# Kernel tuning notes

Measured on AMD Instinct MI355X. Metric: run time of the kernel, lower is better.

The kernel has to match this reference:

```python
import jax, jax.numpy as jnp
import numpy as np

B, T, D, H, K, V = 2, 2048, 2048, 16, 128, 128


def _l2norm(x, eps=1e-12):
    # F.normalize(p=2, dim=-1)
    n = jnp.sqrt(jnp.sum(x * x, axis=-1, keepdims=True))
    return x / jnp.maximum(n, eps)


def setup_inputs() -> dict:
    key = jax.random.key(0)
    ks = jax.random.split(key, 7)
    s = D ** -0.5
    return {
        "x": jax.random.normal(ks[0], (B, T, D), jnp.float32),
        "Wq": jax.random.normal(ks[1], (H * K, D), jnp.float32) * s,
        "Wk": jax.random.normal(ks[2], (H * K, D), jnp.float32) * s,
        "Wv": jax.random.normal(ks[3], (H * V, D), jnp.float32) * s,
        "Wa": jax.random.normal(ks[4], (H, D), jnp.float32) * s,
        "ba": jnp.zeros((H,), jnp.float32),
        "Wb": jax.random.normal(ks[5], (H, D), jnp.float32) * s,
        "bb": jnp.zeros((H,), jnp.float32),
    }


def _forward(x, Wq, Wk, Wv, Wa, ba, Wb, bb):
    Bq, Tq, _ = x.shape
    # projections (nn.Linear: y = x @ W.T)
    q = _l2norm(jnp.einsum('btd,od->bto', x, Wq).reshape(Bq, Tq, H, K))
    k = _l2norm(jnp.einsum('btd,od->bto', x, Wk).reshape(Bq, Tq, H, K))
    v = jnp.einsum('btd,od->bto', x, Wv).reshape(Bq, Tq, H, V)
    alpha = jax.nn.sigmoid(jnp.einsum('btd,hd->bth', x, Wa) + ba)          # [B,T,H] decay in (0,1)
    beta = jax.nn.softplus(jnp.einsum('btd,hd->bth', x, Wb) + bb) * K ** (-0.5)

    # gated delta rule recurrence over time (vectorized over B,H):
    #   S_t = a_t * S_{t-1} (I - b_t k_t k_t^T) + b_t v_t k_t^T ;  o_t = S_t q_t
    def step(S, inp):
        q_t, k_t, v_t, a_t, b_t = inp  # [B,H,K],[B,H,K],[B,H,V],[B,H],[B,H]
        Sd = S * a_t[..., None, None]                              # decay  [B,H,V,K]
        pred = jnp.einsum('bhvk,bhk->bhv', Sd, k_t)                # S k
        u = b_t[..., None] * (v_t - pred)                          # delta update [B,H,V]
        S_new = Sd + u[..., None] * k_t[:, :, None, :]             # rank-1 write
        o_t = jnp.einsum('bhvk,bhk->bhv', S_new, q_t)
        return S_new, o_t

    S0 = jnp.zeros((Bq, H, V, K), x.dtype)
    xs = (q.transpose(1, 0, 2, 3), k.transpose(1, 0, 2, 3),
          v.transpose(1, 0, 2, 3), alpha.transpose(1, 0, 2), beta.transpose(1, 0, 2))
    _, o = jax.lax.scan(step, S0, xs)
    return o.transpose(1, 0, 2, 3)  # [B,T,H,V]


def reference(x, Wq, Wk, Wv, Wa, ba, Wb, bb):
    return _forward(x, Wq, Wk, Wv, Wa, ba, Wb, bb)
```

## Files before the change

kernel.cpp:

```cpp
#include <hip/hip_runtime.h>
#include <math.h>

#define BB 2
#define TT 2048
#define DD 2048
#define HH 16
#define KK 128

typedef _Float16 h4 __attribute__((ext_vector_type(4)));
typedef _Float16 v8h __attribute__((ext_vector_type(8)));
typedef float v4f __attribute__((ext_vector_type(4)));
typedef float f2 __attribute__((ext_vector_type(2)));
typedef unsigned int u2v __attribute__((ext_vector_type(2)));

__global__ __launch_bounds__(256) void gemm_nt3(const float* __restrict__ A,
                                                const float* __restrict__ W0,
                                                const float* __restrict__ W1,
                                                const float* __restrict__ W2,
                                                float* __restrict__ Cbase,
                                                int M, int N, int Kd) {
  __shared__ float As[8][128];
  __shared__ float Bs[8][128];
  const int z = blockIdx.z;
  const float* W = (z == 0) ? W0 : (z == 1) ? W1 : W2;
  float* C = Cbase + (size_t)z * M * N;
  const int tid = threadIdx.x;
  const int bm = blockIdx.y * 128;
  const int bn = blockIdx.x * 128;
  const int lrow = tid >> 1;
  const int lcol = (tid & 1) * 4;
  const int rm = (tid >> 4) * 8;
  const int rn = (tid & 15) * 8;
  const float* Ap = A + (size_t)(bm + lrow) * Kd + lcol;
  const float* Wp = W + (size_t)(bn + lrow) * Kd + lcol;
  float acc[8][8];
#pragma unroll
  for (int i = 0; i < 8; i++)
#pragma unroll
    for (int j = 0; j < 8; j++) acc[i][j] = 0.f;
  float4 av = *(const float4*)Ap;
  float4 wv = *(const float4*)Wp;
  for (int d0 = 0; d0 < Kd; d0 += 8) {
    __syncthreads();
    As[lcol + 0][lrow] = av.x; As[lcol + 1][lrow] = av.y;
    As[lcol + 2][lrow] = av.z; As[lcol + 3][lrow] = av.w;
    Bs[lcol + 0][lrow] = wv.x; Bs[lcol + 1][lrow] = wv.y;
    Bs[lcol + 2][lrow] = wv.z; Bs[lcol + 3][lrow] = wv.w;
    __syncthreads();
    if (d0 + 8 < Kd) {
      av = *(const float4*)(Ap + d0 + 8);
      wv = *(const float4*)(Wp + d0 + 8);
    }
#pragma unroll
    for (int kk = 0; kk < 8; kk++) {
      const float4 a0 = *(const float4*)&As[kk][rm];
      const float4 a1 = *(const float4*)&As[kk][rm + 4];
      const float4 b0 = *(const float4*)&Bs[kk][rn];
      const float4 b1 = *(const float4*)&Bs[kk][rn + 4];
      const float ar[8] = {a0.x, a0.y, a0.z, a0.w, a1.x, a1.y, a1.z, a1.w};
      const float br[8] = {b0.x, b0.y, b0.z, b0.w, b1.x, b1.y, b1.z, b1.w};
#pragma unroll
      for (int i = 0; i < 8; i++)
#pragma unroll
        for (int j = 0; j < 8; j++) acc[i][j] = fmaf(ar[i], br[j], acc[i][j]);
    }
  }
#pragma unroll
  for (int i = 0; i < 8; i++) {
    float* cp = C + (size_t)(bm + rm + i) * N + bn + rn;
    float4 c0 = {acc[i][0], acc[i][1], acc[i][2], acc[i][3]};
    float4 c1 = {acc[i][4], acc[i][5], acc[i][6], acc[i][7]};
    *(float4*)cp = c0;
    *(float4*)(cp + 4) = c1;
  }
}

__global__ __launch_bounds__(256) void convert_f16(
    const float* __restrict__ x, const float* __restrict__ Wq,
    const float* __restrict__ Wk, const float* __restrict__ Wv,
    _Float16* __restrict__ xh, _Float16* __restrict__ Wf) {
  const size_t N4X = (size_t)BB * TT * DD / 4;
  const size_t N4W = (size_t)(HH * KK) * DD / 4;
  const size_t i = (size_t)blockIdx.x * 256 + threadIdx.x;
  if (i < N4X) {
    const float4 v = ((const float4*)x)[i];
    h4 hi;
    hi.x = (_Float16)v.x; hi.y = (_Float16)v.y;
    hi.z = (_Float16)v.z; hi.w = (_Float16)v.w;
    ((h4*)xh)[i] = hi;
  } else {
    const size_t j = i - N4X;
    const float* Ws = (j < N4W) ? Wq : (j < 2 * N4W) ? Wk : Wv;
    const size_t jj = (j < N4W) ? j : (j < 2 * N4W) ? (j - N4W) : (j - 2 * N4W);
    const float4 v = ((const float4*)Ws)[jj];
    h4 hi;
    hi.x = (_Float16)v.x; hi.y = (_Float16)v.y;
    hi.z = (_Float16)v.z; hi.w = (_Float16)v.w;
    ((h4*)Wf)[j] = hi;
  }
}

#define GLDS(gp, lp)                                              \
  __builtin_amdgcn_global_load_lds(                               \
      (const __attribute__((address_space(1))) void*)(gp),        \
      (__attribute__((address_space(3))) void*)(lp), 16, 0, 0)

__global__ __launch_bounds__(256) void gemm_mfma(
    const _Float16* __restrict__ xh, const _Float16* __restrict__ Wf,
    float* __restrict__ Cbase) {
  __shared__ float4 lraw[1024];
  _Float16* Ah = (_Float16*)lraw;
  _Float16* Bs = Ah + 4096;

  const int z = blockIdx.z;
  const _Float16* W = Wf + (size_t)z * DD * (HH * KK);
  float* C = Cbase + (size_t)z * (BB * TT) * (HH * KK);

  const int tid = threadIdx.x;
  const int w = tid >> 6;
  const int lane = tid & 63;
  const int bm = blockIdx.y * 128;
  const int bn = blockIdx.x * 128;
  const int wm = (w & 1) * 64;
  const int wn = (w >> 1) * 64;
  const int m16 = lane & 15;
  const int quad = lane >> 4;

  const _Float16* gA = xh + (size_t)(bm + (tid >> 2)) * DD + (tid & 3) * 8;
  const _Float16* gB = W + (size_t)(bn + (tid >> 2)) * DD + (tid & 3) * 8;
  const int lb = w * 512;

  v4f acc[4][4];
#pragma unroll
  for (int i = 0; i < 4; i++)
#pragma unroll
    for (int j = 0; j < 4; j++) acc[i][j] = (v4f){0.f, 0.f, 0.f, 0.f};

  for (int d0 = 0; d0 < DD; d0 += 32) {
    GLDS(gA + d0, Ah + lb);
    GLDS(gA + d0 + 64 * DD, Ah + 2048 + lb);
    GLDS(gB + d0, Bs + lb);
    GLDS(gB + d0 + 64 * DD, Bs + 2048 + lb);
    __syncthreads();
    v8h ah[4], bw[4];
#pragma unroll
    for (int i = 0; i < 4; i++) {
      ah[i] = *(const v8h*)&Ah[(wm + i * 16 + m16) * 32 + quad * 8];
      bw[i] = *(const v8h*)&Bs[(wn + i * 16 + m16) * 32 + quad * 8];
    }
#pragma unroll
    for (int mi = 0; mi < 4; mi++)
#pragma unroll
      for (int ni = 0; ni < 4; ni++)
        acc[mi][ni] = __builtin_amdgcn_mfma_f32_16x16x32_f16(ah[mi], bw[ni],
                                                             acc[mi][ni], 0, 0, 0);
    __syncthreads();
  }
#pragma unroll
  for (int mi = 0; mi < 4; mi++) {
#pragma unroll
    for (int r = 0; r < 4; r++) {
      float* cp =
          C + (size_t)(bm + wm + mi * 16 + quad * 4 + r) * (HH * KK) + bn + wn + m16;
#pragma unroll
      for (int ni = 0; ni < 4; ni++) cp[ni * 16] = acc[mi][ni][r];
    }
  }
}

__global__ __launch_bounds__(64) void ab_proj(const float* __restrict__ x,
                                              const float* __restrict__ Wa,
                                              const float* __restrict__ ba,
                                              const float* __restrict__ Wb,
                                              const float* __restrict__ bb,
                                              float* __restrict__ abq) {
  const int row = blockIdx.x;
  const int g = blockIdx.y;
  const int h0 = (g & 1) * 8;
  const bool isA = (g < 2);
  const float* W = isA ? Wa : Wb;
  const int lane = threadIdx.x;
  const float* xr = x + (size_t)row * DD;
  float acc[8];
#pragma unroll
  for (int j = 0; j < 8; j++) acc[j] = 0.f;
  for (int d = lane; d < DD; d += 64) {
    const float xv = xr[d];
#pragma unroll
    for (int j = 0; j < 8; j++)
      acc[j] = fmaf(xv, W[(size_t)(h0 + j) * DD + d], acc[j]);
  }
#pragma unroll
  for (int j = 0; j < 8; j++) {
#pragma unroll
    for (int off = 32; off > 0; off >>= 1) acc[j] += __shfl_xor(acc[j], off, 64);
  }
  if (lane == 0) {
    if (isA) {
#pragma unroll
      for (int j = 0; j < 8; j++) {
        const float z = acc[j] + ba[h0 + j];
        abq[((size_t)row * HH + h0 + j) * 4 + 0] = 1.0f / (1.0f + expf(-z));
      }
    } else {
#pragma unroll
      for (int j = 0; j < 8; j++) {
        const float z = acc[j] + bb[h0 + j];
        const float sp = (z > 20.f) ? z : log1pf(expf(z));
        abq[((size_t)row * HH + h0 + j) * 4 + 1] = sp * 0.08838834764831845f;
      }
    }
  }
}

__global__ __launch_bounds__(256) void norm_qk(float* __restrict__ q,
                                               float* __restrict__ k,
                                               float* __restrict__ abq) {
  const int vec = blockIdx.x * 4 + (threadIdx.x >> 6);
  const int l = threadIdx.x & 63;
  float* qp = q + (size_t)vec * 128;
  float* kp = k + (size_t)vec * 128;
  float q0 = qp[l], q1 = qp[l + 64];
  float k0 = kp[l], k1 = kp[l + 64];
  float sq = q0 * q0 + q1 * q1;
  float sk = k0 * k0 + k1 * k1;
#pragma unroll
  for (int off = 32; off > 0; off >>= 1) {
    sq += __shfl_xor(sq, off, 64);
    sk += __shfl_xor(sk, off, 64);
  }
  const float iq = 1.0f / fmaxf(sqrtf(sq), 1e-12f);
  const float ik = 1.0f / fmaxf(sqrtf(sk), 1e-12f);
  q0 *= iq; q1 *= iq; k0 *= ik; k1 *= ik;
  qp[l] = q0; qp[l + 64] = q1;
  kp[l] = k0; kp[l + 64] = k1;
  float pq = q0 * k0 + q1 * k1;
#pragma unroll
  for (int off = 32; off > 0; off >>= 1) pq += __shfl_xor(pq, off, 64);
  if (l == 0) abq[(size_t)vec * 4 + 2] = pq;
}

#define DPP_ADD(x, ctrl)                                                     \
  ((x) + __int_as_float(__builtin_amdgcn_update_dpp(                         \
             0, __float_as_int(x), (ctrl), 0xF, 0xF, true)))

__device__ __forceinline__ float xadd32(float x) {
  const u2v r = __builtin_amdgcn_permlane32_swap(__float_as_uint(x),
                                                 __float_as_uint(x), false,
                                                 false);
  return __uint_as_float(r.x) + __uint_as_float(r.y);
}

#define SBAR() asm volatile("s_barrier" ::: "memory")
#define WAITV(n) asm volatile("s_waitcnt vmcnt(" #n ")" ::: "memory")

#define SCAN_MATH(kc, qc, vc, ac, jj, obname)                                  \
  {                                                                            \
    const f2 ka = {kc.x, kc.y};                                                \
    const f2 kb2 = {kc.z, kc.w};                                               \
    const f2 qa = {qc.x, qc.y};                                                \
    const f2 qb2 = {qc.z, qc.w};                                               \
    const f2 pdk = __builtin_elementwise_fma(Sb, kb2, Sa * ka);                \
    const f2 pdq = __builtin_elementwise_fma(Sb, qb2, Sa * qa);                \
    float dk = pdk.x + pdk.y;                                                  \
    float dq = pdq.x + pdq.y;                                                  \
    dk = DPP_ADD(dk, 0xB1);  dq = DPP_ADD(dq, 0xB1);             \
    dk = DPP_ADD(dk, 0x4E);  dq = DPP_ADD(dq, 0x4E);             \
    dk = DPP_ADD(dk, 0x141); dq = DPP_ADD(dq, 0x141);            \
    dk = DPP_ADD(dk, 0x140); dq = DPP_ADD(dq, 0x140);            \
    dk = xadd32(dk);         dq = xadd32(dq);                    \
    const float u = ac.y * fmaf(-ac.x, dk, vc);                                \
    const float oo = fmaf(ac.x, dq, u * ac.z);                                 \
    const f2 a2 = {ac.x, ac.x};                                                \
    const f2 u2 = {u, u};                                                      \
    Sa = __builtin_elementwise_fma(a2, Sa, u2 * ka);                           \
    Sb = __builtin_elementwise_fma(a2, Sb, u2 * kb2);                          \
    obname = (ks == (jj)) ? oo : obname;                                       \
  }

#define STAGE(bi, tg)                                                          \
  {                                                                            \
    const float* gk =                                                          \
        kU + (size_t)((tg) + 2 * w + (lane >> 5)) * 2048 + (lane & 31) * 4;    \
    GLDS(gk, &Kb[bi][2 * w][0]);                                               \
    const float* gq =                                                          \
        qU + (size_t)((tg) + 2 * w + (lane >> 5)) * 2048 + (lane & 31) * 4;    \
    GLDS(gq, &Qb[bi][2 * w][0]);                                               \
    if (lane < 8) GLDS(aU + (size_t)((tg) + lane) * 64, &Ab[bi][0][0]);        \
    _Pragma("unroll") for (int jj = 0; jj < 8; jj++)                           \
        vf##bi[jj] = vU[vrow + (size_t)((tg) + jj) * 2048];                    \
  }

#define COMPUTE_GROUP(bi, obname)                                              \
  float obname = 0.f;                                                          \
  _Pragma("unroll") for (int j = 0; j < 8; j++) {                              \
    const float4 kc = *(const float4*)&Kb[bi][j][ks4];                         \
    const float4 qc = *(const float4*)&Qb[bi][j][ks4];                         \
    const float4 ac = *(const float4*)&Ab[bi][j][0];                           \
    const float vc = vf##bi[j];                                                \
    SCAN_MATH(kc, qc, vc, ac, j, obname);                                      \
  }

__global__ __launch_bounds__(256, 2) void scan_kernel(
    const float* __restrict__ q, const float* __restrict__ k,
    const float* __restrict__ v, const float* __restrict__ abq,
    float* __restrict__ o) {
  __shared__ float Kb[2][8][128];
  __shared__ float Qb[2][8][128];
  __shared__ float Ab[2][8][4];

  const int bid = blockIdx.x;
  const int bh = bid & 31;
  const int s = bid >> 5;
  const int h = bh & 15;
  const int b = bh >> 4;
  const int tid = threadIdx.x;
  const int w = tid >> 6;
  const int lane = tid & 63;
  const int rg = (lane >> 4) & 1;
  const int ks = (lane & 15) | ((lane >> 5) << 4);
  const int ks4 = ks * 4;
  const int vrow = s * 8 + w * 2 + rg;

  const size_t base = (size_t)b * TT * 2048 + (size_t)h * KK;
  const float* kU = k + base;
  const float* qU = q + base;
  const float* vU = v + base;
  const float* aU = abq + ((size_t)b * TT * HH + h) * 4;
  float* oU = o + base;

  f2 Sa = {0.f, 0.f}, Sb = {0.f, 0.f};
  float vf0[8], vf1[8];

  STAGE(0, 0);
  STAGE(1, 8);
  WAITV(11);
  SBAR();
  __builtin_amdgcn_sched_barrier(0);

  int tg = 0;
  for (int gp = 0; gp < TT / 8; gp += 2) {
    COMPUTE_GROUP(0, ob0);
    if (ks < 8) oU[vrow + (size_t)(tg + ks) * 2048] = ob0;
    SBAR();
    if (gp + 2 < TT / 8) {
      STAGE(0, tg + 16);
      WAITV(11);
    } else {
      WAITV(0);
    }
    SBAR();
    __builtin_amdgcn_sched_barrier(0);

    COMPUTE_GROUP(1, ob1);
    if (ks < 8) oU[vrow + (size_t)(tg + 8 + ks) * 2048] = ob1;
    SBAR();
    if (gp + 3 < TT / 8) {
      STAGE(1, tg + 24);
      WAITV(11);
    } else {
      WAITV(0);
    }
    SBAR();
    __builtin_amdgcn_sched_barrier(0);

    tg += 16;
  }
}

extern "C" void kernel_launch(void* const* d_in, const int* in_sizes, int n_in,
                              void* d_out, int out_size, void* d_ws,
                              size_t ws_size, hipStream_t stream) {
  const float* x = (const float*)d_in[0];
  const float* Wq = (const float*)d_in[1];
  const float* Wk = (const float*)d_in[2];
  const float* Wv = (const float*)d_in[3];
  const float* Wa = (const float*)d_in[4];
  const float* ba = (const float*)d_in[5];
  const float* Wb = (const float*)d_in[6];
  const float* bb = (const float*)d_in[7];
  float* out = (float*)d_out;
  float* ws = (float*)d_ws;

  const size_t PROJ = (size_t)BB * TT * HH * KK;
  const size_t NABQ = (size_t)BB * TT * HH * 4;
  float* qw = ws;
  float* kw = ws + PROJ;
  float* vw = ws + 2 * PROJ;
  float* abq = ws + 3 * PROJ;
  _Float16* xh = (_Float16*)(abq + NABQ);
  _Float16* Wf = xh + (size_t)BB * TT * DD;
  const size_t NEED = (3 * PROJ + NABQ) * 4 +
                      ((size_t)BB * TT * DD + 3 * (size_t)(HH * KK) * DD) * 2;

  const int M = BB * TT;
  const int N = HH * KK;
  if (ws_size >= NEED) {
    const int cgrid = (int)(((size_t)BB * TT * DD / 4 + 3 * (size_t)N * DD / 4) / 256);
    convert_f16<<<cgrid, 256, 0, stream>>>(x, Wq, Wk, Wv, xh, Wf);
    gemm_mfma<<<dim3(N / 128, M / 128, 3), 256, 0, stream>>>(xh, Wf, qw);
  } else {
    gemm_nt3<<<dim3(N / 128, M / 128, 3), 256, 0, stream>>>(x, Wq, Wk, Wv, qw,
                                                            M, N, DD);
  }
  ab_proj<<<dim3(M, 4), 64, 0, stream>>>(x, Wa, ba, Wb, bb, abq);
  norm_qk<<<(BB * TT * HH) / 4, 256, 0, stream>>>(qw, kw, abq);
  scan_kernel<<<BB * HH * 16, 256, 0, stream>>>(qw, kw, vw, abq, out);
}
```

Measured before the change: 720.6 us.

## Replace sequential delta-rule scan with chunked WY-form scan (prep + chunk scan)

Adds a chunk-parallel formulation of the gated delta rule. A prep kernel computes per-32-step chunk decay factors, the intra-chunk Gram matrices, a triangular inverse T, and T·(beta·v), with one chunk per block in parallel. A second kernel then walks the 64 chunks per head, with 8 blocks per head each owning 16 value rows, and updates the state once per chunk rather than once per step. It also merges the four ab_proj blocks per row into one 256-thread block. The cost is extra workspace traffic and a fallback path when the workspace is too small, plus numerical risk from the exp2/log2 cumulative decays.

```diff
diff --git a/kernel.cpp b/kernel.cpp
--- a/kernel.cpp
+++ b/kernel.cpp
@@ -168,18 +168,18 @@
   }
 }
 
-__global__ __launch_bounds__(64) void ab_proj(const float* __restrict__ x,
-                                              const float* __restrict__ Wa,
-                                              const float* __restrict__ ba,
-                                              const float* __restrict__ Wb,
-                                              const float* __restrict__ bb,
-                                              float* __restrict__ abq) {
+__global__ __launch_bounds__(256) void ab_proj(const float* __restrict__ x,
+                                               const float* __restrict__ Wa,
+                                               const float* __restrict__ ba,
+                                               const float* __restrict__ Wb,
+                                               const float* __restrict__ bb,
+                                               float* __restrict__ abq) {
   const int row = blockIdx.x;
-  const int g = blockIdx.y;
+  const int g = threadIdx.x >> 6;
+  const int lane = threadIdx.x & 63;
   const int h0 = (g & 1) * 8;
   const bool isA = (g < 2);
   const float* W = isA ? Wa : Wb;
-  const int lane = threadIdx.x;
   const float* xr = x + (size_t)row * DD;
   float acc[8];
 #pragma unroll
@@ -237,7 +237,11 @@
   float pq = q0 * k0 + q1 * k1;
 #pragma unroll
   for (int off = 32; off > 0; off >>= 1) pq += __shfl_xor(pq, off, 64);
-  if (l == 0) abq[(size_t)vec * 4 + 2] = pq;
+  if (l == 0) {
+    abq[(size_t)vec * 4 + 2] = pq;
+    abq[(size_t)vec * 4 + 3] =
+        abq[(size_t)vec * 4 + 0] * abq[(size_t)vec * 4 + 1];
+  }
 }
 
 #define DPP_ADD(x, ctrl)                                                     \
@@ -264,11 +268,11 @@
     const f2 pdq = __builtin_elementwise_fma(Sb, qb2, Sa * qa);                \
     float dk = pdk.x + pdk.y;                                                  \
     float dq = pdq.x + pdq.y;                                                  \
-    dk = DPP_ADD(dk, 0xB1);  dq = DPP_ADD(dq, 0xB1);             \
-    dk = DPP_ADD(dk, 0x4E);  dq = DPP_ADD(dq, 0x4E);             \
-    dk = DPP_ADD(dk, 0x141); dq = DPP_ADD(dq, 0x141);            \
-    dk = DPP_ADD(dk, 0x140); dq = DPP_ADD(dq, 0x140);            \
-    dk = xadd32(dk);         dq = xadd32(dq);                    \
+    dk = DPP_ADD(dk, 0xB1);  dq = DPP_ADD(dq, 0xB1);                           \
+    dk = DPP_ADD(dk, 0x4E);  dq = DPP_ADD(dq, 0x4E);                           \
+    dk = DPP_ADD(dk, 0x141); dq = DPP_ADD(dq, 0x141);                          \
+    dk = DPP_ADD(dk, 0x140); dq = DPP_ADD(dq, 0x140);                          \
+    dk = xadd32(dk);         dq = xadd32(dq);                                  \
     const float u = ac.y * fmaf(-ac.x, dk, vc);                                \
     const float oo = fmaf(ac.x, dq, u * ac.z);                                 \
     const f2 a2 = {ac.x, ac.x};                                                \
@@ -365,6 +369,246 @@
     __builtin_amdgcn_sched_barrier(0);
 
     tg += 16;
+  }
+}
+
+__global__ __launch_bounds__(64) void chunk_prep(
+    const float* __restrict__ q, const float* __restrict__ k,
+    const float* __restrict__ v, const float* __restrict__ abq,
+    float* __restrict__ cT2, float* __restrict__ cMq,
+    float* __restrict__ cTbv, float* __restrict__ cgv,
+    float* __restrict__ cwv, float* __restrict__ cgC) {
+  __shared__ float Ks[32][132];
+  __shared__ float Qs[32][132];
+  __shared__ float G[32][33];
+  __shared__ float Gq[32][33];
+  __shared__ float Tm[32][33];
+  __shared__ float la[32], lg[32], bs_[32];
+
+  const int c = blockIdx.x;
+  const int b = c >> 10, h = (c >> 6) & 15, ci = c & 63;
+  const int l = threadIdx.x;
+  const size_t rowbase = (size_t)b * TT + ci * 32;
+
+#pragma unroll
+  for (int seg = 0; seg < 16; ++seg) {
+    const int idx = l + 64 * seg;
+    const int r = idx >> 5, cq = (idx & 31) * 4;
+    const size_t g = (rowbase + r) * 2048 + (size_t)h * KK + cq;
+    *(float4*)&Ks[r][cq] = *(const float4*)&k[g];
+    *(float4*)&Qs[r][cq] = *(const float4*)&q[g];
+  }
+  if (l < 32) {
+    const size_t ar = ((rowbase + l) * HH + h) * 4;
+    la[l] = log2f(abq[ar]);
+    bs_[l] = abq[ar + 1];
+  }
+  __syncthreads();
+  if (l < 32) {
+    float s = 0.f;
+    for (int r = 0; r <= l; ++r) s += la[r];
+    lg[l] = s;
+  }
+  __syncthreads();
+  const float lgC = lg[31];
+  for (int p = l; p < 1024; p += 64) {
+    const int s = p >> 5, r = p & 31;
+    float aK = 0.f, aQ = 0.f;
+#pragma unroll
+    for (int kk2 = 0; kk2 < 128; kk2 += 4) {
+      const float4 kr = *(const float4*)&Ks[r][kk2];
+      const float4 ks2 = *(const float4*)&Ks[s][kk2];
+      const float4 qs2 = *(const float4*)&Qs[s][kk2];
+      aK = fmaf(kr.x, ks2.x, fmaf(kr.y, ks2.y, fmaf(kr.z, ks2.z, fmaf(kr.w, ks2.w, aK))));
+      aQ = fmaf(kr.x, qs2.x, fmaf(kr.y, qs2.y, fmaf(kr.z, qs2.z, fmaf(kr.w, qs2.w, aQ))));
+    }
+    G[s][r] = aK;
+    Gq[s][r] = aQ;
+  }
+  __syncthreads();
+  for (int p = l; p < 1024; p += 64) {
+    const int s = p >> 5, r = p & 31;
+    const float ratio = exp2f(lg[s] - lg[r]);
+    const float Lv = (r < s) ? bs_[s] * ratio * G[s][r] : 0.f;
+    const float Mv = (r <= s) ? ratio * Gq[s][r] : 0.f;
+    G[s][r] = Lv;
+    cMq[(size_t)c * 1024 + s * 32 + r] = Mv;
+  }
+  __syncthreads();
+  if (l < 32) {
+    for (int s = 0; s < 32; ++s) {
+      float acc = 0.f;
+      for (int r = 0; r < s; ++r) acc = fmaf(G[s][r], Tm[r][l], acc);
+      Tm[s][l] = ((l == s) ? 1.f : 0.f) - acc;
+      asm volatile("s_waitcnt lgkmcnt(0)" ::: "memory");
+    }
+  }
+  __syncthreads();
+  for (int p = l; p < 1024; p += 64) {
+    const int s = p >> 5, r = p & 31;
+    cT2[(size_t)c * 1024 + s * 32 + r] = Tm[s][r] * (bs_[r] * exp2f(lg[r]));
+  }
+  if (l < 32) {
+    cgv[(size_t)c * 32 + l] = exp2f(lg[l]);
+    cwv[(size_t)c * 32 + l] = exp2f(lgC - lg[l]);
+    if (l == 0) cgC[c] = exp2f(lgC);
+  }
+  __syncthreads();
+#pragma unroll
+  for (int seg = 0; seg < 16; ++seg) {
+    const int idx = l + 64 * seg;
+    const int r = idx >> 5, cq = (idx & 31) * 4;
+    const size_t g = (rowbase + r) * 2048 + (size_t)h * KK + cq;
+    float4 vv = *(const float4*)&v[g];
+    const float br = bs_[r];
+    vv.x *= br; vv.y *= br; vv.z *= br; vv.w *= br;
+    *(float4*)&Ks[r][cq] = vv;
+  }
+  __syncthreads();
+  if (l < 32) {
+    for (int ib = 0; ib < 8; ++ib) {
+      float4 a0 = {0, 0, 0, 0}, a1 = {0, 0, 0, 0};
+      float4 a2 = {0, 0, 0, 0}, a3 = {0, 0, 0, 0};
+      for (int r = 0; r < 32; ++r) {
+        const float tmr = Tm[l][r];
+        const float4 v0 = *(const float4*)&Ks[r][ib * 16 + 0];
+        const float4 v1 = *(const float4*)&Ks[r][ib * 16 + 4];
+        const float4 v2 = *(const float4*)&Ks[r][ib * 16 + 8];
+        const float4 v3 = *(const float4*)&Ks[r][ib * 16 + 12];
+        a0.x = fmaf(tmr, v0.x, a0.x); a0.y = fmaf(tmr, v0.y, a0.y);
+        a0.z = fmaf(tmr, v0.z, a0.z); a0.w = fmaf(tmr, v0.w, a0.w);
+        a1.x = fmaf(tmr, v1.x, a1.x); a1.y = fmaf(tmr, v1.y, a1.y);
+        a1.z = fmaf(tmr, v1.z, a1.z); a1.w = fmaf(tmr, v1.w, a1.w);
+        a2.x = fmaf(tmr, v2.x, a2.x); a2.y = fmaf(tmr, v2.y, a2.y);
+        a2.z = fmaf(tmr, v2.z, a2.z); a2.w = fmaf(tmr, v2.w, a2.w);
+        a3.x = fmaf(tmr, v3.x, a3.x); a3.y = fmaf(tmr, v3.y, a3.y);
+        a3.z = fmaf(tmr, v3.z, a3.z); a3.w = fmaf(tmr, v3.w, a3.w);
+      }
+      float* dst = &cTbv[(size_t)c * 4096 + l * 128 + ib * 16];
+      *(float4*)(dst + 0) = a0;
+      *(float4*)(dst + 4) = a1;
+      *(float4*)(dst + 8) = a2;
+      *(float4*)(dst + 12) = a3;
+    }
+  }
+}
+
+__global__ __launch_bounds__(256) void chunk_scan(
+    const float* __restrict__ q, const float* __restrict__ k,
+    const float* __restrict__ cT2, const float* __restrict__ cMq,
+    const float* __restrict__ cTbv, const float* __restrict__ cgv,
+    const float* __restrict__ cwv, const float* __restrict__ cgC,
+    float* __restrict__ o) {
+  __shared__ float Ss[16][132];
+  __shared__ float Ks[32][132];
+  __shared__ float Qs[32][132];
+  __shared__ float Ps[16][33];
+  __shared__ float Pqs[16][33];
+  __shared__ float Us[32][17];
+  __shared__ float T2s[32][36];
+  __shared__ float Mqs[32][36];
+  __shared__ float Tbs[32][20];
+  __shared__ float gv[32], wv[32];
+
+  const int blk = blockIdx.x;
+  const int head = blk >> 3, vb = blk & 7;
+  const int b = head >> 4, h = head & 15;
+  const int vb0 = vb * 16;
+  const int t = threadIdx.x;
+
+  for (int i = t; i < 16 * 132; i += 256) ((float*)Ss)[i] = 0.f;
+
+  const int sU = t & 31, ipU = t >> 5;
+  const int i0 = 2 * ipU, i1 = i0 + 1;
+  const int iO = t & 15, tr0 = (t >> 4) * 2;
+  const int iS = t >> 4, kb = (t & 15) * 8;
+
+  for (int ci = 0; ci < 64; ++ci) {
+    const int c = (head << 6) + ci;
+    const size_t rowbase = (size_t)b * TT + ci * 32;
+    __syncthreads();
+#pragma unroll
+    for (int seg = 0; seg < 4; ++seg) {
+      const int idx = t + 256 * seg;
+      const int r = idx >> 5, cq = (idx & 31) * 4;
+      const size_t g = (rowbase + r) * 2048 + (size_t)h * KK + cq;
+      *(float4*)&Ks[r][cq] = *(const float4*)&k[g];
+      *(float4*)&Qs[r][cq] = *(const float4*)&q[g];
+    }
+    {
+      const int r = t >> 3, cq = (t & 7) * 4;
+      *(float4*)&T2s[r][cq] = *(const float4*)&cT2[(size_t)c * 1024 + r * 32 + cq];
+      *(float4*)&Mqs[r][cq] = *(const float4*)&cMq[(size_t)c * 1024 + r * 32 + cq];
+    }
+    if (t < 128) {
+      const int r = t >> 2, cq = (t & 3) * 4;
+      *(float4*)&Tbs[r][cq] =
+          *(const float4*)&cTbv[(size_t)c * 4096 + r * 128 + vb0 + cq];
+    }
+    if (t < 32) {
+      gv[t] = cgv[(size_t)c * 32 + t];
+      wv[t] = cwv[(size_t)c * 32 + t];
+    }
+    const float gc = cgC[c];
+    __syncthreads();
+    {
+      float p0 = 0.f, p1 = 0.f, pq0 = 0.f, pq1 = 0.f;
+#pragma unroll
+      for (int kk2 = 0; kk2 < 128; kk2 += 4) {
+        const float4 s0 = *(const float4*)&Ss[i0][kk2];
+        const float4 s1 = *(const float4*)&Ss[i1][kk2];
+        const float4 kv = *(const float4*)&Ks[sU][kk2];
+        const float4 qv = *(const float4*)&Qs[sU][kk2];
+        p0 = fmaf(s0.x, kv.x, fmaf(s0.y, kv.y, fmaf(s0.z, kv.z, fmaf(s0.w, kv.w, p0))));
+        p1 = fmaf(s1.x, kv.x, fmaf(s1.y, kv.y, fmaf(s1.z, kv.z, fmaf(s1.w, kv.w, p1))));
+        pq0 = fmaf(s0.x, qv.x, fmaf(s0.y, qv.y, fmaf(s0.z, qv.z, fmaf(s0.w, qv.w, pq0))));
+        pq1 = fmaf(s1.x, qv.x, fmaf(s1.y, qv.y, fmaf(s1.z, qv.z, fmaf(s1.w, qv.w, pq1))));
+      }
+      Ps[i0][sU] = p0; Ps[i1][sU] = p1;
+      Pqs[i0][sU] = pq0; Pqs[i1][sU] = pq1;
+    }
+    __syncthreads();
+    {
+      float u0 = Tbs[sU][i0], u1 = Tbs[sU][i1];
+#pragma unroll
+      for (int r = 0; r < 32; ++r) {
+        const float t2 = T2s[sU][r];
+        u0 = fmaf(-t2, Ps[i0][r], u0);
+        u1 = fmaf(-t2, Ps[i1][r], u1);
+      }
+      Us[sU][i0] = u0; Us[sU][i1] = u1;
+    }
+    __syncthreads();
+    {
+      float o0 = gv[tr0] * Pqs[iO][tr0];
+      float o1 = gv[tr0 + 1] * Pqs[iO][tr0 + 1];
+#pragma unroll
+      for (int s2 = 0; s2 < 32; ++s2) {
+        const float uu = Us[s2][iO];
+        o0 = fmaf(Mqs[tr0][s2], uu, o0);
+        o1 = fmaf(Mqs[tr0 + 1][s2], uu, o1);
+      }
+      const size_t og = (rowbase + tr0) * 2048 + (size_t)h * KK + vb0 + iO;
+      o[og] = o0;
+      o[og + 2048] = o1;
+    }
+    {
+      float acc[8];
+#pragma unroll
+      for (int j = 0; j < 8; ++j) acc[j] = gc * Ss[iS][kb + j];
+#pragma unroll
+      for (int s2 = 0; s2 < 32; ++s2) {
+        const float cw = wv[s2] * Us[s2][iS];
+        const float4 k0 = *(const float4*)&Ks[s2][kb];
+        const float4 k1 = *(const float4*)&Ks[s2][kb + 4];
+        acc[0] = fmaf(cw, k0.x, acc[0]); acc[1] = fmaf(cw, k0.y, acc[1]);
+        acc[2] = fmaf(cw, k0.z, acc[2]); acc[3] = fmaf(cw, k0.w, acc[3]);
+        acc[4] = fmaf(cw, k1.x, acc[4]); acc[5] = fmaf(cw, k1.y, acc[5]);
+        acc[6] = fmaf(cw, k1.z, acc[6]); acc[7] = fmaf(cw, k1.w, acc[7]);
+      }
+#pragma unroll
+      for (int j = 0; j < 8; ++j) Ss[iS][kb + j] = acc[j];
+    }
   }
 }
 
@@ -390,8 +634,17 @@
   float* abq = ws + 3 * PROJ;
   _Float16* xh = (_Float16*)(abq + NABQ);
   _Float16* Wf = xh + (size_t)BB * TT * DD;
+  float* cT2 = (float*)(Wf + 3 * (size_t)(HH * KK) * DD);
+  float* cMq = cT2 + (size_t)2048 * 1024;
+  float* cTbv = cMq + (size_t)2048 * 1024;
+  float* cgv = cTbv + (size_t)2048 * 4096;
+  float* cwv = cgv + (size_t)2048 * 32;
+  float* cgC = cwv + (size_t)2048 * 32;
+
   const size_t NEED = (3 * PROJ + NABQ) * 4 +
                       ((size_t)BB * TT * DD + 3 * (size_t)(HH * KK) * DD) * 2;
+  const size_t NEED2 =
+      NEED + ((size_t)2048 * 1024 * 2 + (size_t)2048 * 4096 + 2048 * 64 + 2048) * 4;
 
   const int M = BB * TT;
   const int N = HH * KK;
@@ -403,7 +656,14 @@
     gemm_nt3<<<dim3(N / 128, M / 128, 3), 256, 0, stream>>>(x, Wq, Wk, Wv, qw,
                                                             M, N, DD);
   }
-  ab_proj<<<dim3(M, 4), 64, 0, stream>>>(x, Wa, ba, Wb, bb, abq);
+  ab_proj<<<M, 256, 0, stream>>>(x, Wa, ba, Wb, bb, abq);
   norm_qk<<<(BB * TT * HH) / 4, 256, 0, stream>>>(qw, kw, abq);
-  scan_kernel<<<BB * HH * 16, 256, 0, stream>>>(qw, kw, vw, abq, out);
-}
+  if (ws_size >= NEED2) {
+    chunk_prep<<<2048, 64, 0, stream>>>(qw, kw, vw, abq, cT2, cMq, cTbv, cgv,
+                                        cwv, cgC);
+    chunk_scan<<<256, 256, 0, stream>>>(qw, kw, cT2, cMq, cTbv, cgv, cwv, cgC,
+                                        out);
+  } else {
+    scan_kernel<<<BB * HH * 16, 256, 0, stream>>>(qw, kw, vw, abq, out);
+  }
+}
```

After: 860.0 us. 19.3% more time.
